# Kernel optimization log

Hardware: AMD Instinct MI355X
Metric: run time of the kernel (lower is better)

The kernel has to match this reference:

```python
import jax, jax.numpy as jnp
import numpy as np

MODES_X = 16
MODES_Y = 16


def setup_inputs() -> dict:
    key = jax.random.key(0)
    ks = jax.random.split(key, 8)
    B, H, W, C = 32, 128, 128, 64
    scale = 1.0 / (C * C)
    x = jax.random.normal(ks[0], (B, H, W, C), dtype=jnp.float32)
    w1_real = scale * jax.random.normal(ks[1], (MODES_X, MODES_Y, C, C), dtype=jnp.float32)
    w1_imag = scale * jax.random.normal(ks[2], (MODES_X, MODES_Y, C, C), dtype=jnp.float32)
    w2_real = scale * jax.random.normal(ks[3], (MODES_X, MODES_Y, C, C), dtype=jnp.float32)
    w2_imag = scale * jax.random.normal(ks[4], (MODES_X, MODES_Y, C, C), dtype=jnp.float32)
    dense_kernel = jax.random.normal(ks[5], (C, C), dtype=jnp.float32) / np.sqrt(C)
    dense_bias = jnp.zeros((C,), dtype=jnp.float32)
    return {"x": x, "w1_real": w1_real, "w1_imag": w1_imag,
            "w2_real": w2_real, "w2_imag": w2_imag,
            "dense_kernel": dense_kernel, "dense_bias": dense_bias}


def _spectral_conv2d(x, w1, w2, mx, my):
    # x: [B,H,W,C] real; w1,w2: [mx,my,C,C] complex
    B, H, W, C = x.shape
    x_ft = jnp.fft.rfft2(x, axes=(1, 2))  # [B,H,W//2+1,C] complex64
    out_ft = jnp.zeros((B, H, W // 2 + 1, C), dtype=x_ft.dtype)
    # low positive x-frequencies
    out_ft = out_ft.at[:, :mx, :my].set(
        jnp.einsum('bxyi,xyio->bxyo', x_ft[:, :mx, :my], w1))
    # low negative x-frequencies
    out_ft = out_ft.at[:, -mx:, :my].set(
        jnp.einsum('bxyi,xyio->bxyo', x_ft[:, -mx:, :my], w2))
    return jnp.fft.irfft2(out_ft, s=(H, W), axes=(1, 2))


def reference(x, w1_real, w1_imag, w2_real, w2_imag, dense_kernel, dense_bias):
    w1 = w1_real + 1j * w1_imag
    w2 = w2_real + 1j * w2_imag
    y_s = _spectral_conv2d(x, w1, w2, MODES_X, MODES_Y)
    y_p = jnp.einsum('bhwi,io->bhwo', x, dense_kernel) + dense_bias
    return jax.nn.gelu(x + y_s + y_p, approximate=True)
```

## Files before the change

### kernel.cpp

```cpp
#include <hip/hip_runtime.h>
#include <math.h>

#define BB 32
#define HH 128
#define WW 128
#define CC 64
#define MX 16
#define MY 16
#define NKX 32

#define TWOPI 6.283185307179586f

typedef __attribute__((ext_vector_type(8))) short bf16x8;
typedef __attribute__((ext_vector_type(4))) float f32x4;

__device__ inline unsigned short f2bf(float f) {
    union { float f; unsigned u; } v; v.f = f;
    unsigned r = v.u + 0x7FFFu + ((v.u >> 16) & 1u);
    return (unsigned short)(r >> 16);
}


__global__ __launch_bounds__(256) void kT(const float* __restrict__ K, unsigned short* __restrict__ FR) {
    __shared__ float2 tw[128];
    int tid = threadIdx.x;
    if (tid < 128) {
        float s, c;
        sincosf(TWOPI * (float)tid * (1.0f / 128.0f), &s, &c);
        tw[tid] = make_float2(c, s);
    }
    __syncthreads();
    int g = blockIdx.x * 256 + tid;
    short v[8];
    if (g < 512) {
        int s = g;
        int l = s & 63, ks = (s >> 6) & 3, mt = s >> 8;
        int q = l >> 4, r = l & 15;
        int row = mt * 16 + r, ky = row >> 1, ri = row & 1;
        int k0 = ks * 32 + q * 8;
        #pragma unroll
        for (int e = 0; e < 8; ++e) {
            float2 t = tw[(ky * (k0 + e)) & 127];
            v[e] = (short)f2bf(ri ? -t.y : t.x);
        }
    } else if (g < 2560) {
        int s = g - 512;
        int l = s & 63, ks = (s >> 6) & 7, mt = s >> 9;
        int q = l >> 4, r = l & 15;
        int row = mt * 16 + r, kxi = row >> 1, rr = row & 1;
        int kx = (kxi < 16) ? kxi : (96 + kxi);
        int k0 = ks * 32 + q * 8;
        #pragma unroll
        for (int e = 0; e < 8; ++e) {
            int k = k0 + e, h = k >> 1, ri = k & 1;
            float2 t = tw[(kx * h) & 127];
            float val = (rr == 0) ? (ri == 0 ? t.x : t.y) : (ri == 0 ? -t.y : t.x);
            v[e] = (short)f2bf(val);
        }
    } else if (g < 3584) {
        int s = g - 2560;
        int l = s & 63, ks = (s >> 6) & 1, mt = s >> 7;
        int q = l >> 4, r = l & 15;
        int h = mt * 16 + r;
        int k0 = ks * 32 + q * 8;
        #pragma unroll
        for (int e = 0; e < 8; ++e) {
            int k = k0 + e, kxi = k >> 1, ri = k & 1;
            int kx = (kxi < 16) ? kxi : (96 + kxi);
            float2 t = tw[(kx * h) & 127];
            v[e] = (short)f2bf(ri == 0 ? t.x : -t.y);
        }
    } else if (g < 4096) {
        int s = g - 3584;
        int l = s & 63, tm = s >> 6;
        int q = l >> 4, r = l & 15;
        int row = tm * 16 + r;
        const float inv = 1.0f / 16384.0f;
        #pragma unroll
        for (int e = 0; e < 8; ++e) {
            int ky = 4 * q + (e >> 1);
            float sc = ((ky == 0) ? 1.0f : 2.0f) * inv;
            float2 t = tw[(ky * row) & 127];
            v[e] = (short)f2bf((e & 1) ? (-t.y * sc) : (t.x * sc));
        }
    } else {
        int s = g - 4096;
        int l = s & 63, ks = (s >> 6) & 1, nt = s >> 7;
        int q = l >> 4, r = l & 15;
        int col = nt * 16 + r;
        #pragma unroll
        for (int e = 0; e < 8; ++e) {
            int k = ks * 32 + q * 8 + e;
            v[e] = (short)f2bf(K[k * CC + col]);
        }
    }
    *(bf16x8*)&FR[(size_t)g * 8] = *(const bf16x8*)v;
}

__global__ __launch_bounds__(256) void kA(const float* __restrict__ x, const unsigned short* __restrict__ FR,
                                          unsigned short* __restrict__ X1) {
    __shared__ unsigned short xbf[WW * CC];
    int tid = threadIdx.x, bh = blockIdx.x;
    const float* xp = x + (size_t)bh * (WW * CC);
    for (int i = tid * 4; i < WW * CC; i += 1024) {
        float4 v = *(const float4*)&xp[i];
        ushort4 pk = make_ushort4(f2bf(v.x), f2bf(v.y), f2bf(v.z), f2bf(v.w));
        *(ushort4*)&xbf[i] = pk;
    }
    __syncthreads();
    int lane = tid & 63, nt = tid >> 6, q = lane >> 4, r = lane & 15;
    bf16x8 bfv[4];
    #pragma unroll
    for (int ks = 0; ks < 4; ++ks) {
        short v[8];
        #pragma unroll
        for (int e = 0; e < 8; ++e)
            v[e] = (short)xbf[(ks * 32 + q * 8 + e) * CC + nt * 16 + r];
        bfv[ks] = *(const bf16x8*)v;
    }
    f32x4 acc0 = {0.f, 0.f, 0.f, 0.f}, acc1 = {0.f, 0.f, 0.f, 0.f};
    #pragma unroll
    for (int ks = 0; ks < 4; ++ks) {
        bf16x8 a0 = *(const bf16x8*)&FR[((size_t)((0 * 4 + ks) * 64 + lane)) * 8];
        bf16x8 a1 = *(const bf16x8*)&FR[((size_t)((1 * 4 + ks) * 64 + lane)) * 8];
        acc0 = __builtin_amdgcn_mfma_f32_16x16x32_bf16(a0, bfv[ks], acc0, 0, 0, 0);
        acc1 = __builtin_amdgcn_mfma_f32_16x16x32_bf16(a1, bfv[ks], acc1, 0, 0, 0);
    }
    __syncthreads();
    unsigned short* asT = xbf;
    int c = nt * 16 + r;
    #pragma unroll
    for (int j = 0; j < 4; ++j) {
        int m0 = q * 4 + j;
        asT[m0 * 64 + c] = f2bf(acc0[j]);
        asT[(16 + m0) * 64 + c] = f2bf(acc1[j]);
    }
    __syncthreads();
    int b = bh >> 7, h = bh & 127;
    int ky = tid >> 4, idx8 = tid & 15;
    int ri = idx8 >> 3, c0 = (idx8 & 7) * 8;
    bf16x8 vv = *(const bf16x8*)&asT[(2 * ky + ri) * 64 + c0];
    *(bf16x8*)&X1[(((size_t)b * 16 + ky) * 128 + h) * 128 + ri * 64 + c0] = vv;
}

__global__ __launch_bounds__(256) void kB(const unsigned short* __restrict__ X1, const unsigned short* __restrict__ FR,
                                          unsigned short* __restrict__ X2) {
    __shared__ unsigned short xb[256 * 64];
    int tid = threadIdx.x, blk = blockIdx.x;
    int b = blk >> 4, ky = blk & 15;
    const unsigned short* p = X1 + ((size_t)b * 16 + ky) * 16384;
    for (int i = tid * 8; i < 256 * 64; i += 2048)
        *(bf16x8*)&xb[i] = *(const bf16x8*)&p[i];
    __syncthreads();
    const unsigned short* FB = FR + 4096;
    int lane = tid & 63, wid = tid >> 6, q = lane >> 4, r = lane & 15;
    int col = wid * 16 + r;
    bf16x8 bfv[8];
    #pragma unroll
    for (int ks = 0; ks < 8; ++ks) {
        short v[8];
        #pragma unroll
        for (int e = 0; e < 8; ++e)
            v[e] = (short)xb[(ks * 32 + q * 8 + e) * 64 + col];
        bfv[ks] = *(const bf16x8*)v;
    }
    f32x4 acc[4] = {{0.f,0.f,0.f,0.f},{0.f,0.f,0.f,0.f},{0.f,0.f,0.f,0.f},{0.f,0.f,0.f,0.f}};
    #pragma unroll
    for (int ks = 0; ks < 8; ++ks) {
        #pragma unroll
        for (int mt = 0; mt < 4; ++mt) {
            bf16x8 a = *(const bf16x8*)&FB[((size_t)((mt * 8 + ks) * 64 + lane)) * 8];
            acc[mt] = __builtin_amdgcn_mfma_f32_16x16x32_bf16(a, bfv[ks], acc[mt], 0, 0, 0);
        }
    }
    __syncthreads();
    unsigned short* asT = xb;
    #pragma unroll
    for (int mt = 0; mt < 4; ++mt)
        #pragma unroll
        for (int j = 0; j < 4; ++j)
            asT[(mt * 16 + q * 4 + j) * 64 + col] = f2bf(acc[mt][j]);
    __syncthreads();
    int kxi = tid >> 3, part = tid & 7;
    short v2[16];
    #pragma unroll
    for (int s = 0; s < 16; ++s) {
        int n = part * 16 + s, cc2 = n >> 1, rr = n & 1;
        v2[s] = (short)asT[(2 * kxi + rr) * 64 + cc2];
    }
    unsigned short* dst = &X2[(((size_t)b * NKX + kxi) * 16 + ky) * 128 + part * 16];
    *(bf16x8*)&dst[0] = *(const bf16x8*)&v2[0];
    *(bf16x8*)&dst[8] = *(const bf16x8*)&v2[8];
}

__global__ __launch_bounds__(256) void kC(const float* __restrict__ w1r, const float* __restrict__ w1i,
                                          const float* __restrict__ w2r, const float* __restrict__ w2i,
                                          const unsigned short* __restrict__ X2, unsigned short* __restrict__ G) {
    __shared__ unsigned short wbr[CC * CC];
    __shared__ unsigned short wbi[CC * CC];
    __shared__ unsigned short asT[32 * 128];
    int tid = threadIdx.x;
    int blk = blockIdx.x;
    int kxi = blk >> 4, ky = blk & 15;
    const float* wr = (kxi < 16) ? w1r : w2r;
    const float* wi = (kxi < 16) ? w1i : w2i;
    int wx = (kxi < 16) ? kxi : (kxi - 16);
    size_t woff = ((size_t)wx * MY + ky) * (CC * CC);
    for (int i = tid * 4; i < CC * CC; i += 1024) {
        float4 a = *(const float4*)&wr[woff + i];
        float4 bq = *(const float4*)&wi[woff + i];
        *(ushort4*)&wbr[i] = make_ushort4(f2bf(a.x), f2bf(a.y), f2bf(a.z), f2bf(a.w));
        *(ushort4*)&wbi[i] = make_ushort4(f2bf(bq.x), f2bf(bq.y), f2bf(bq.z), f2bf(bq.w));
    }
    __syncthreads();

    int lane = tid & 63, wid = tid >> 6;
    int q = lane >> 4, r = lane & 15;
    bf16x8 af[2][4];
    #pragma unroll
    for (int mt = 0; mt < 2; ++mt) {
        int b = mt * 16 + r;
        #pragma unroll
        for (int ks = 0; ks < 4; ++ks)
            af[mt][ks] = *(const bf16x8*)&X2[(((size_t)b * NKX + kxi) * 16 + ky) * 128 + ks * 32 + q * 8];
    }
    bf16x8 bfr[2][4];
    #pragma unroll
    for (int t = 0; t < 2; ++t) {
        int n = (wid * 2 + t) * 16 + r;
        int o = n >> 1, ro = n & 1;
        #pragma unroll
        for (int ks = 0; ks < 4; ++ks) {
            short v[8];
            #pragma unroll
            for (int e = 0; e < 8; ++e) {
                int k = ks * 32 + q * 8 + e;
                int i = k >> 1, ri = k & 1;
                unsigned short raw = (ri == 0) ? (ro ? wbi[i * 64 + o] : wbr[i * 64 + o])
                                               : (ro ? wbr[i * 64 + o] : (unsigned short)(wbi[i * 64 + o] ^ 0x8000u));
                v[e] = (short)raw;
            }
            bfr[t][ks] = *(const bf16x8*)v;
        }
    }
    f32x4 acc[2][2] = {{{0.f,0.f,0.f,0.f},{0.f,0.f,0.f,0.f}},{{0.f,0.f,0.f,0.f},{0.f,0.f,0.f,0.f}}};
    #pragma unroll
    for (int ks = 0; ks < 4; ++ks)
        #pragma unroll
        for (int mt = 0; mt < 2; ++mt)
            #pragma unroll
            for (int t = 0; t < 2; ++t)
                acc[mt][t] = __builtin_amdgcn_mfma_f32_16x16x32_bf16(af[mt][ks], bfr[t][ks], acc[mt][t], 0, 0, 0);
    #pragma unroll
    for (int mt = 0; mt < 2; ++mt)
        #pragma unroll
        for (int t = 0; t < 2; ++t)
            #pragma unroll
            for (int j = 0; j < 4; ++j)
                asT[(mt * 16 + q * 4 + j) * 128 + (wid * 2 + t) * 16 + r] = f2bf(acc[mt][t][j]);
    __syncthreads();
    int bb = tid >> 3, part = tid & 7;
    bf16x8 u0 = *(const bf16x8*)&asT[bb * 128 + part * 16];
    bf16x8 u1 = *(const bf16x8*)&asT[bb * 128 + part * 16 + 8];
    unsigned short* dst = &G[(((size_t)bb * NKX + kxi) * 16 + ky) * 128 + part * 16];
    *(bf16x8*)&dst[0] = u0;
    *(bf16x8*)&dst[8] = u1;
}

__global__ __launch_bounds__(256) void kD(const unsigned short* __restrict__ G, const unsigned short* __restrict__ FR,
                                          unsigned short* __restrict__ Zf) {
    __shared__ unsigned short gs[NKX * 128];
    int tid = threadIdx.x, blk = blockIdx.x;
    int b = blk >> 5, ky = (blk >> 1) & 15, mh = blk & 1;
    for (int i = tid * 8; i < NKX * 128; i += 2048) {
        int kxi = i >> 7, n = i & 127;
        *(bf16x8*)&gs[i] = *(const bf16x8*)&G[(((size_t)b * NKX + kxi) * 16 + ky) * 128 + n];
    }
    __syncthreads();
    int lane = tid & 63, wid = tid >> 6, q = lane >> 4, r = lane & 15;
    const unsigned short* FD = FR + 20480;
    bf16x8 bfr[2][2];
    #pragma unroll
    for (int t = 0; t < 2; ++t) {
        int n = (wid * 2 + t) * 16 + r;
        #pragma unroll
        for (int ks = 0; ks < 2; ++ks) {
            short v[8];
            #pragma unroll
            for (int e = 0; e < 8; ++e) {
                int k = ks * 32 + q * 8 + e;
                int kxi = k >> 1, ri = k & 1;
                unsigned short raw = gs[kxi * 128 + (n ^ ri)];
                if (ri & (n & 1)) raw ^= 0x8000u;
                v[e] = (short)raw;
            }
            bfr[t][ks] = *(const bf16x8*)v;
        }
    }
    #pragma unroll
    for (int mt2 = 0; mt2 < 4; ++mt2) {
        int mt = mh * 4 + mt2;
        f32x4 acc[2] = {{0.f,0.f,0.f,0.f},{0.f,0.f,0.f,0.f}};
        #pragma unroll
        for (int ks = 0; ks < 2; ++ks) {
            bf16x8 a = *(const bf16x8*)&FD[((size_t)((mt * 2 + ks) * 64 + lane)) * 8];
            #pragma unroll
            for (int t = 0; t < 2; ++t)
                acc[t] = __builtin_amdgcn_mfma_f32_16x16x32_bf16(a, bfr[t][ks], acc[t], 0, 0, 0);
        }
        #pragma unroll
        for (int t = 0; t < 2; ++t)
            #pragma unroll
            for (int j = 0; j < 4; ++j) {
                int h = mt * 16 + q * 4 + j;
                int n = (wid * 2 + t) * 16 + r;
                int c = n >> 1, reim = n & 1;
                int kp = 2 * ky + reim, q2 = kp >> 3, e2 = kp & 7;
                int nt2 = c >> 4, r2 = c & 15;
                Zf[(((size_t)b * 128 + h) * 4 + nt2) * 512 + (q2 * 16 + r2) * 8 + e2] = f2bf(acc[t][j]);
            }
    }
}

__global__ __launch_bounds__(256) void kE(const float* __restrict__ x, const unsigned short* __restrict__ Zf,
                                          const unsigned short* __restrict__ FR,
                                          const float* __restrict__ bias, float* __restrict__ out) {
    __shared__ float xs[WW * 68];
    int tid = threadIdx.x, bh = blockIdx.x;
    const float* xp = x + (size_t)bh * (WW * CC);
    for (int i = tid * 4; i < WW * CC; i += 1024) {
        int w = i >> 6, c = i & 63;
        *(float4*)&xs[w * 68 + c] = *(const float4*)&xp[i];
    }
    __syncthreads();
    int lane = tid & 63, wv = tid >> 6, q = lane >> 4, r = lane & 15;
    const unsigned short* FEAT = FR + 28672;
    const unsigned short* FEBK = FR + 32768;
    bf16x8 ax[2][2], at[2];
    #pragma unroll
    for (int t2 = 0; t2 < 2; ++t2) {
        int tm = wv * 2 + t2;
        int row = tm * 16 + r;
        #pragma unroll
        for (int ks = 0; ks < 2; ++ks) {
            const float* s = &xs[row * 68 + ks * 32 + q * 8];
            short v[8];
            #pragma unroll
            for (int e = 0; e < 8; ++e) v[e] = (short)f2bf(s[e]);
            ax[t2][ks] = *(const bf16x8*)v;
        }
        at[t2] = *(const bf16x8*)&FEAT[((size_t)(tm * 64 + lane)) * 8];
    }
    #pragma unroll
    for (int nt = 0; nt < 4; ++nt) {
        bf16x8 b0 = *(const bf16x8*)&FEBK[((size_t)((nt * 2 + 0) * 64 + lane)) * 8];
        bf16x8 b1 = *(const bf16x8*)&FEBK[((size_t)((nt * 2 + 1) * 64 + lane)) * 8];
        bf16x8 bz = *(const bf16x8*)&Zf[((size_t)bh * 4 + nt) * 512 + lane * 8];
        int c = nt * 16 + r;
        float bsv = bias[c];
        #pragma unroll
        for (int t2 = 0; t2 < 2; ++t2) {
            int tm = wv * 2 + t2;
            f32x4 acc = {0.f, 0.f, 0.f, 0.f};
            acc = __builtin_amdgcn_mfma_f32_16x16x32_bf16(ax[t2][0], b0, acc, 0, 0, 0);
            acc = __builtin_amdgcn_mfma_f32_16x16x32_bf16(ax[t2][1], b1, acc, 0, 0, 0);
            acc = __builtin_amdgcn_mfma_f32_16x16x32_bf16(at[t2], bz, acc, 0, 0, 0);
            #pragma unroll
            for (int j = 0; j < 4; ++j) {
                int w = tm * 16 + q * 4 + j;
                float u = acc[j] + xs[w * 68 + c] + bsv;
                float t = u + 0.044715f * u * u * u;
                float e = __expf(-1.5957691216057308f * t);
                out[(size_t)bh * (WW * CC) + w * CC + c] = u / (1.0f + e);
            }
        }
    }
}

extern "C" void kernel_launch(void* const* d_in, const int* in_sizes, int n_in,
                              void* d_out, int out_size, void* d_ws, size_t ws_size,
                              hipStream_t stream) {
    const float* x   = (const float*)d_in[0];
    const float* w1r = (const float*)d_in[1];
    const float* w1i = (const float*)d_in[2];
    const float* w2r = (const float*)d_in[3];
    const float* w2i = (const float*)d_in[4];
    const float* dk  = (const float*)d_in[5];
    const float* db  = (const float*)d_in[6];
    float* out = (float*)d_out;

    unsigned short* FR = (unsigned short*)d_ws;
    unsigned short* X1 = FR + 65536;
    unsigned short* X2 = X1 + 8388608;
    unsigned short* G  = X2 + 2097152;
    unsigned short* Zf = G  + 2097152;

    kT<<<18, 256, 0, stream>>>(dk, FR);
    kA<<<BB * HH, 256, 0, stream>>>(x, FR, X1);
    kB<<<BB * MY, 256, 0, stream>>>(X1, FR, X2);
    kC<<<NKX * MY, 256, 0, stream>>>(w1r, w1i, w2r, w2i, X2, G);
    kD<<<BB * MY * 2, 256, 0, stream>>>(G, FR, Zf);
    kE<<<BB * HH, 256, 0, stream>>>(x, Zf, FR, db, out);
}
```

Measured before the change: 328.4 us.

## Fuse five stage kernels into one cooperative persistent kernel with grid syncs

Replaces the five back-to-back launches (kA through kE) with a single cooperative kernel of 1024 blocks that runs each stage in turn, separated by grid.sync barriers. Stages that had 4096 blocks now loop over four rows per block, and a fallback path runs the old kernels if the cooperative launch fails. The goal is to remove per-launch overhead and the tail idle time between kernels. The cost is that half the blocks sit idle in the 512-block stages, occupancy is capped at four blocks per CU, and grid-wide barriers carry their own expense.

```diff
diff --git a/kernel.cpp b/kernel.cpp
--- a/kernel.cpp
+++ b/kernel.cpp
@@ -1,4 +1,5 @@
 #include <hip/hip_runtime.h>
+#include <hip/hip_cooperative_groups.h>
 #include <math.h>
 
 #define BB 32
@@ -10,6 +11,8 @@
 #define NKX 32
 
 #define TWOPI 6.283185307179586f
+
+namespace cg = cooperative_groups;
 
 typedef __attribute__((ext_vector_type(8))) short bf16x8;
 typedef __attribute__((ext_vector_type(4))) float f32x4;
@@ -97,6 +100,300 @@
     *(bf16x8*)&FR[(size_t)g * 8] = *(const bf16x8*)v;
 }
 
+__global__ __launch_bounds__(256, 4) void kFused(
+        const float* __restrict__ x,
+        const float* __restrict__ w1r, const float* __restrict__ w1i,
+        const float* __restrict__ w2r, const float* __restrict__ w2i,
+        const float* __restrict__ bias,
+        const unsigned short* __restrict__ FR,
+        unsigned short* __restrict__ X1, unsigned short* __restrict__ X2,
+        unsigned short* __restrict__ G, unsigned short* __restrict__ Zf,
+        float* __restrict__ out) {
+    cg::grid_group grid = cg::this_grid();
+    __shared__ __align__(16) char smem[34816];
+    int tid = threadIdx.x, blk = blockIdx.x;
+    int lane = tid & 63, wid = tid >> 6, q = lane >> 4, r = lane & 15;
+
+    {
+        unsigned short* xbf = (unsigned short*)smem;
+        #pragma unroll 1
+        for (int u = 0; u < 4; ++u) {
+            int bh = blk * 4 + u;
+            __syncthreads();
+            const float* xp = x + (size_t)bh * (WW * CC);
+            for (int i = tid * 4; i < WW * CC; i += 1024) {
+                float4 v = *(const float4*)&xp[i];
+                *(ushort4*)&xbf[i] = make_ushort4(f2bf(v.x), f2bf(v.y), f2bf(v.z), f2bf(v.w));
+            }
+            __syncthreads();
+            int nt = wid;
+            bf16x8 bfv[4];
+            #pragma unroll
+            for (int ks = 0; ks < 4; ++ks) {
+                short v[8];
+                #pragma unroll
+                for (int e = 0; e < 8; ++e)
+                    v[e] = (short)xbf[(ks * 32 + q * 8 + e) * CC + nt * 16 + r];
+                bfv[ks] = *(const bf16x8*)v;
+            }
+            f32x4 acc0 = {0.f, 0.f, 0.f, 0.f}, acc1 = {0.f, 0.f, 0.f, 0.f};
+            #pragma unroll
+            for (int ks = 0; ks < 4; ++ks) {
+                bf16x8 a0 = *(const bf16x8*)&FR[((size_t)((0 * 4 + ks) * 64 + lane)) * 8];
+                bf16x8 a1 = *(const bf16x8*)&FR[((size_t)((1 * 4 + ks) * 64 + lane)) * 8];
+                acc0 = __builtin_amdgcn_mfma_f32_16x16x32_bf16(a0, bfv[ks], acc0, 0, 0, 0);
+                acc1 = __builtin_amdgcn_mfma_f32_16x16x32_bf16(a1, bfv[ks], acc1, 0, 0, 0);
+            }
+            __syncthreads();
+            unsigned short* asT = xbf;
+            int c = nt * 16 + r;
+            #pragma unroll
+            for (int j = 0; j < 4; ++j) {
+                int m0 = q * 4 + j;
+                asT[m0 * 64 + c] = f2bf(acc0[j]);
+                asT[(16 + m0) * 64 + c] = f2bf(acc1[j]);
+            }
+            __syncthreads();
+            int b = bh >> 7, h = bh & 127;
+            int ky = tid >> 4, idx8 = tid & 15;
+            int ri = idx8 >> 3, c0 = (idx8 & 7) * 8;
+            bf16x8 vv = *(const bf16x8*)&asT[(2 * ky + ri) * 64 + c0];
+            *(bf16x8*)&X1[(((size_t)b * 16 + ky) * 128 + h) * 128 + ri * 64 + c0] = vv;
+        }
+    }
+    __threadfence();
+    grid.sync();
+
+    if (blk < 512) {
+        unsigned short* xb = (unsigned short*)smem;
+        int b = blk >> 4, ky = blk & 15;
+        const unsigned short* p = X1 + ((size_t)b * 16 + ky) * 16384;
+        for (int i = tid * 8; i < 256 * 64; i += 2048)
+            *(bf16x8*)&xb[i] = *(const bf16x8*)&p[i];
+        __syncthreads();
+        const unsigned short* FB = FR + 4096;
+        int col = wid * 16 + r;
+        bf16x8 bfv[8];
+        #pragma unroll
+        for (int ks = 0; ks < 8; ++ks) {
+            short v[8];
+            #pragma unroll
+            for (int e = 0; e < 8; ++e)
+                v[e] = (short)xb[(ks * 32 + q * 8 + e) * 64 + col];
+            bfv[ks] = *(const bf16x8*)v;
+        }
+        f32x4 acc[4] = {{0.f,0.f,0.f,0.f},{0.f,0.f,0.f,0.f},{0.f,0.f,0.f,0.f},{0.f,0.f,0.f,0.f}};
+        #pragma unroll
+        for (int ks = 0; ks < 8; ++ks) {
+            #pragma unroll
+            for (int mt = 0; mt < 4; ++mt) {
+                bf16x8 a = *(const bf16x8*)&FB[((size_t)((mt * 8 + ks) * 64 + lane)) * 8];
+                acc[mt] = __builtin_amdgcn_mfma_f32_16x16x32_bf16(a, bfv[ks], acc[mt], 0, 0, 0);
+            }
+        }
+        __syncthreads();
+        unsigned short* asT = xb;
+        #pragma unroll
+        for (int mt = 0; mt < 4; ++mt)
+            #pragma unroll
+            for (int j = 0; j < 4; ++j)
+                asT[(mt * 16 + q * 4 + j) * 64 + col] = f2bf(acc[mt][j]);
+        __syncthreads();
+        int kxi = tid >> 3, part = tid & 7;
+        short v2[16];
+        #pragma unroll
+        for (int s = 0; s < 16; ++s) {
+            int n = part * 16 + s, cc2 = n >> 1, rr = n & 1;
+            v2[s] = (short)asT[(2 * kxi + rr) * 64 + cc2];
+        }
+        unsigned short* dst = &X2[(((size_t)b * NKX + kxi) * 16 + ky) * 128 + part * 16];
+        *(bf16x8*)&dst[0] = *(const bf16x8*)&v2[0];
+        *(bf16x8*)&dst[8] = *(const bf16x8*)&v2[8];
+    }
+    __threadfence();
+    grid.sync();
+
+    if (blk < 512) {
+        unsigned short* wbr = (unsigned short*)smem;
+        unsigned short* wbi = wbr + CC * CC;
+        unsigned short* asT = wbi + CC * CC;
+        int kxi = blk >> 4, ky = blk & 15;
+        const float* wr = (kxi < 16) ? w1r : w2r;
+        const float* wi = (kxi < 16) ? w1i : w2i;
+        int wx = (kxi < 16) ? kxi : (kxi - 16);
+        size_t woff = ((size_t)wx * MY + ky) * (CC * CC);
+        for (int i = tid * 4; i < CC * CC; i += 1024) {
+            float4 a = *(const float4*)&wr[woff + i];
+            float4 bq = *(const float4*)&wi[woff + i];
+            *(ushort4*)&wbr[i] = make_ushort4(f2bf(a.x), f2bf(a.y), f2bf(a.z), f2bf(a.w));
+            *(ushort4*)&wbi[i] = make_ushort4(f2bf(bq.x), f2bf(bq.y), f2bf(bq.z), f2bf(bq.w));
+        }
+        __syncthreads();
+        bf16x8 af[2][4];
+        #pragma unroll
+        for (int mt = 0; mt < 2; ++mt) {
+            int b = mt * 16 + r;
+            #pragma unroll
+            for (int ks = 0; ks < 4; ++ks)
+                af[mt][ks] = *(const bf16x8*)&X2[(((size_t)b * NKX + kxi) * 16 + ky) * 128 + ks * 32 + q * 8];
+        }
+        bf16x8 bfr[2][4];
+        #pragma unroll
+        for (int t = 0; t < 2; ++t) {
+            int n = (wid * 2 + t) * 16 + r;
+            int o = n >> 1, ro = n & 1;
+            #pragma unroll
+            for (int ks = 0; ks < 4; ++ks) {
+                short v[8];
+                #pragma unroll
+                for (int e = 0; e < 8; ++e) {
+                    int k = ks * 32 + q * 8 + e;
+                    int i = k >> 1, ri = k & 1;
+                    unsigned short raw = (ri == 0) ? (ro ? wbi[i * 64 + o] : wbr[i * 64 + o])
+                                                   : (ro ? wbr[i * 64 + o] : (unsigned short)(wbi[i * 64 + o] ^ 0x8000u));
+                    v[e] = (short)raw;
+                }
+                bfr[t][ks] = *(const bf16x8*)v;
+            }
+        }
+        f32x4 acc[2][2] = {{{0.f,0.f,0.f,0.f},{0.f,0.f,0.f,0.f}},{{0.f,0.f,0.f,0.f},{0.f,0.f,0.f,0.f}}};
+        #pragma unroll
+        for (int ks = 0; ks < 4; ++ks)
+            #pragma unroll
+            for (int mt = 0; mt < 2; ++mt)
+                #pragma unroll
+                for (int t = 0; t < 2; ++t)
+                    acc[mt][t] = __builtin_amdgcn_mfma_f32_16x16x32_bf16(af[mt][ks], bfr[t][ks], acc[mt][t], 0, 0, 0);
+        #pragma unroll
+        for (int mt = 0; mt < 2; ++mt)
+            #pragma unroll
+            for (int t = 0; t < 2; ++t)
+                #pragma unroll
+                for (int j = 0; j < 4; ++j)
+                    asT[(mt * 16 + q * 4 + j) * 128 + (wid * 2 + t) * 16 + r] = f2bf(acc[mt][t][j]);
+        __syncthreads();
+        int bb = tid >> 3, part = tid & 7;
+        bf16x8 u0 = *(const bf16x8*)&asT[bb * 128 + part * 16];
+        bf16x8 u1 = *(const bf16x8*)&asT[bb * 128 + part * 16 + 8];
+        unsigned short* dst = &G[(((size_t)bb * NKX + kxi) * 16 + ky) * 128 + part * 16];
+        *(bf16x8*)&dst[0] = u0;
+        *(bf16x8*)&dst[8] = u1;
+    }
+    __threadfence();
+    grid.sync();
+
+    {
+        unsigned short* gs = (unsigned short*)smem;
+        int b = blk >> 5, ky = (blk >> 1) & 15, mh = blk & 1;
+        __syncthreads();
+        for (int i = tid * 8; i < NKX * 128; i += 2048) {
+            int kxi = i >> 7, n = i & 127;
+            *(bf16x8*)&gs[i] = *(const bf16x8*)&G[(((size_t)b * NKX + kxi) * 16 + ky) * 128 + n];
+        }
+        __syncthreads();
+        const unsigned short* FD = FR + 20480;
+        bf16x8 bfr[2][2];
+        #pragma unroll
+        for (int t = 0; t < 2; ++t) {
+            int n = (wid * 2 + t) * 16 + r;
+            #pragma unroll
+            for (int ks = 0; ks < 2; ++ks) {
+                short v[8];
+                #pragma unroll
+                for (int e = 0; e < 8; ++e) {
+                    int k = ks * 32 + q * 8 + e;
+                    int kxi = k >> 1, ri = k & 1;
+                    unsigned short raw = gs[kxi * 128 + (n ^ ri)];
+                    if (ri & (n & 1)) raw ^= 0x8000u;
+                    v[e] = (short)raw;
+                }
+                bfr[t][ks] = *(const bf16x8*)v;
+            }
+        }
+        #pragma unroll
+        for (int mt2 = 0; mt2 < 4; ++mt2) {
+            int mt = mh * 4 + mt2;
+            f32x4 acc[2] = {{0.f,0.f,0.f,0.f},{0.f,0.f,0.f,0.f}};
+            #pragma unroll
+            for (int ks = 0; ks < 2; ++ks) {
+                bf16x8 a = *(const bf16x8*)&FD[((size_t)((mt * 2 + ks) * 64 + lane)) * 8];
+                #pragma unroll
+                for (int t = 0; t < 2; ++t)
+                    acc[t] = __builtin_amdgcn_mfma_f32_16x16x32_bf16(a, bfr[t][ks], acc[t], 0, 0, 0);
+            }
+            #pragma unroll
+            for (int t = 0; t < 2; ++t)
+                #pragma unroll
+                for (int j = 0; j < 4; ++j) {
+                    int h = mt * 16 + q * 4 + j;
+                    int n = (wid * 2 + t) * 16 + r;
+                    int c = n >> 1, reim = n & 1;
+                    int kp = 2 * ky + reim, q2 = kp >> 3, e2 = kp & 7;
+                    int nt2 = c >> 4, r2 = c & 15;
+                    Zf[(((size_t)b * 128 + h) * 4 + nt2) * 512 + (q2 * 16 + r2) * 8 + e2] = f2bf(acc[t][j]);
+                }
+        }
+    }
+    __threadfence();
+    grid.sync();
+
+    {
+        float* xs = (float*)smem;
+        const unsigned short* FEAT = FR + 28672;
+        const unsigned short* FEBK = FR + 32768;
+        #pragma unroll 1
+        for (int u = 0; u < 4; ++u) {
+            int bh = blk * 4 + u;
+            __syncthreads();
+            const float* xp = x + (size_t)bh * (WW * CC);
+            for (int i = tid * 4; i < WW * CC; i += 1024) {
+                int w = i >> 6, c = i & 63;
+                *(float4*)&xs[w * 68 + c] = *(const float4*)&xp[i];
+            }
+            __syncthreads();
+            bf16x8 ax[2][2], at[2];
+            #pragma unroll
+            for (int t2 = 0; t2 < 2; ++t2) {
+                int tm = wid * 2 + t2;
+                int row = tm * 16 + r;
+                #pragma unroll
+                for (int ks = 0; ks < 2; ++ks) {
+                    const float* s = &xs[row * 68 + ks * 32 + q * 8];
+                    short v[8];
+                    #pragma unroll
+                    for (int e = 0; e < 8; ++e) v[e] = (short)f2bf(s[e]);
+                    ax[t2][ks] = *(const bf16x8*)v;
+                }
+                at[t2] = *(const bf16x8*)&FEAT[((size_t)(tm * 64 + lane)) * 8];
+            }
+            #pragma unroll
+            for (int nt = 0; nt < 4; ++nt) {
+                bf16x8 b0 = *(const bf16x8*)&FEBK[((size_t)((nt * 2 + 0) * 64 + lane)) * 8];
+                bf16x8 b1 = *(const bf16x8*)&FEBK[((size_t)((nt * 2 + 1) * 64 + lane)) * 8];
+                bf16x8 bz = *(const bf16x8*)&Zf[((size_t)bh * 4 + nt) * 512 + lane * 8];
+                int c = nt * 16 + r;
+                float bsv = bias[c];
+                #pragma unroll
+                for (int t2 = 0; t2 < 2; ++t2) {
+                    int tm = wid * 2 + t2;
+                    f32x4 acc = {0.f, 0.f, 0.f, 0.f};
+                    acc = __builtin_amdgcn_mfma_f32_16x16x32_bf16(ax[t2][0], b0, acc, 0, 0, 0);
+                    acc = __builtin_amdgcn_mfma_f32_16x16x32_bf16(ax[t2][1], b1, acc, 0, 0, 0);
+                    acc = __builtin_amdgcn_mfma_f32_16x16x32_bf16(at[t2], bz, acc, 0, 0, 0);
+                    #pragma unroll
+                    for (int j = 0; j < 4; ++j) {
+                        int w = tm * 16 + q * 4 + j;
+                        float uu = acc[j] + xs[w * 68 + c] + bsv;
+                        float t = uu + 0.044715f * uu * uu * uu;
+                        float e = __expf(-1.5957691216057308f * t);
+                        out[(size_t)bh * (WW * CC) + w * CC + c] = uu / (1.0f + e);
+                    }
+                }
+            }
+        }
+    }
+}
+
 __global__ __launch_bounds__(256) void kA(const float* __restrict__ x, const unsigned short* __restrict__ FR,
                                           unsigned short* __restrict__ X1) {
     __shared__ unsigned short xbf[WW * CC];
@@ -104,8 +401,7 @@
     const float* xp = x + (size_t)bh * (WW * CC);
     for (int i = tid * 4; i < WW * CC; i += 1024) {
         float4 v = *(const float4*)&xp[i];
-        ushort4 pk = make_ushort4(f2bf(v.x), f2bf(v.y), f2bf(v.z), f2bf(v.w));
-        *(ushort4*)&xbf[i] = pk;
+        *(ushort4*)&xbf[i] = make_ushort4(f2bf(v.x), f2bf(v.y), f2bf(v.z), f2bf(v.w));
     }
     __syncthreads();
     int lane = tid & 63, nt = tid >> 6, q = lane >> 4, r = lane & 15;
@@ -213,7 +509,6 @@
         *(ushort4*)&wbi[i] = make_ushort4(f2bf(bq.x), f2bf(bq.y), f2bf(bq.z), f2bf(bq.w));
     }
     __syncthreads();
-
     int lane = tid & 63, wid = tid >> 6;
     int q = lane >> 4, r = lane & 15;
     bf16x8 af[2][4];
@@ -396,9 +691,23 @@
     unsigned short* Zf = G  + 2097152;
 
     kT<<<18, 256, 0, stream>>>(dk, FR);
-    kA<<<BB * HH, 256, 0, stream>>>(x, FR, X1);
-    kB<<<BB * MY, 256, 0, stream>>>(X1, FR, X2);
-    kC<<<NKX * MY, 256, 0, stream>>>(w1r, w1i, w2r, w2i, X2, G);
-    kD<<<BB * MY * 2, 256, 0, stream>>>(G, FR, Zf);
-    kE<<<BB * HH, 256, 0, stream>>>(x, Zf, FR, db, out);
-}
+
+    const float* xa = x; const float* a1 = w1r; const float* a2 = w1i;
+    const float* a3 = w2r; const float* a4 = w2i; const float* bb = db;
+    const unsigned short* fr = FR;
+    unsigned short* x1 = X1; unsigned short* x2 = X2;
+    unsigned short* gg = G; unsigned short* zf = Zf;
+    float* oo = out;
+    void* args[] = {(void*)&xa, (void*)&a1, (void*)&a2, (void*)&a3, (void*)&a4,
+                    (void*)&bb, (void*)&fr, (void*)&x1, (void*)&x2, (void*)&gg,
+                    (void*)&zf, (void*)&oo};
+    hipError_t err = hipLaunchCooperativeKernel((const void*)kFused, dim3(1024), dim3(256),
+                                                args, 0, stream);
+    if (err != hipSuccess) {
+        kA<<<BB * HH, 256, 0, stream>>>(x, FR, X1);
+        kB<<<BB * MY, 256, 0, stream>>>(X1, FR, X2);
+        kC<<<NKX * MY, 256, 0, stream>>>(w1r, w1i, w2r, w2i, X2, G);
+        kD<<<BB * MY * 2, 256, 0, stream>>>(G, FR, Zf);
+        kE<<<BB * HH, 256, 0, stream>>>(x, Zf, FR, db, out);
+    }
+}
```

New measurement: 1.301 ms. 3.96x slower.
